# Kernel tuning notes

Hardware: AMD Instinct MI355X
Metric: run time of the kernel (lower is better)

The kernel has to match this reference:

```python
import jax, jax.numpy as jnp
import numpy as np

N_EMBD = 1024
HEADS = 16
HEAD_DIM = N_EMBD // HEADS


def setup_inputs() -> dict:
    key = jax.random.key(0)
    k1, k2 = jax.random.split(key)
    x = jax.random.normal(k1, (2, 2048, N_EMBD), dtype=jnp.float32)
    W_qkv = jax.random.normal(k2, (N_EMBD, 3 * N_EMBD), dtype=jnp.float32) * (N_EMBD ** -0.5)
    b_qkv = jnp.zeros((3 * N_EMBD,), dtype=jnp.float32)
    return {"x": x, "W_qkv": W_qkv, "b_qkv": b_qkv}


def reference(x, W_qkv, b_qkv):
    B, T, _ = x.shape
    qkv = x @ W_qkv + b_qkv                      # [B, T, 3*n_embd]
    q, k, v = jnp.split(qkv, 3, axis=-1)
    q = q.reshape(B, T, HEADS, HEAD_DIM)
    k = k.reshape(B, T, HEADS, HEAD_DIM)
    v = v.reshape(B, T, HEADS, HEAD_DIM)
    attn = jnp.einsum('bthd,bThd->bhtT', q, k) / jnp.sqrt(jnp.float32(HEAD_DIM))
    causal = jnp.tril(jnp.ones((T, T), dtype=bool))  # [T, T]
    attn = jnp.where(causal, attn, -jnp.inf)
    attn = jax.nn.softmax(attn, axis=-1)
    # dropout is identity in deterministic/eval mode (training=False)
    out = jnp.einsum('bhtT,bThd->bthd', attn, v).reshape(B, T, N_EMBD)
    return out
```

## Files before the change

### kernel.cpp

```cpp
#include <hip/hip_runtime.h>
#include <hip/hip_bf16.h>

#define BATCH 2
#define TSEQ  2048
#define NEMBD 1024
#define HEADS 16
#define HDIM  64

typedef short          bf16x8 __attribute__((ext_vector_type(8)));
typedef float          f32x4  __attribute__((ext_vector_type(4)));
typedef unsigned short u16;

__device__ __forceinline__ u16 f2bf(float f) {
  unsigned int u = __float_as_uint(f);
  u += 0x7fffu + ((u >> 16) & 1u);
  return (u16)(u >> 16);
}

__device__ __forceinline__ void gld16(const u16* g, u16* l) {
  __builtin_amdgcn_global_load_lds(
      (const __attribute__((address_space(1))) unsigned int*)g,
      (__attribute__((address_space(3))) unsigned int*)l, 16, 0, 0);
}

__global__ __launch_bounds__(256) void k_prep(const float* __restrict__ x,
                                              u16* __restrict__ xb,
                                              const float* __restrict__ w,
                                              u16* __restrict__ wt) {
  __shared__ float tile[32][33];
  const int t = threadIdx.x;
  if (blockIdx.x < 4096) {
    int i = blockIdx.x * 256 + t;
    float4 v = ((const float4*)x)[i];
    ushort4 o;
    o.x = f2bf(v.x); o.y = f2bf(v.y); o.z = f2bf(v.z); o.w = f2bf(v.w);
    ((ushort4*)xb)[i] = o;
    return;
  }
  const int bid = blockIdx.x - 4096;
  const int n0 = (bid % 96) * 32;
  const int k0 = (bid / 96) * 32;
  const int r  = t >> 3;
  const int c4 = (t & 7) * 4;
  float4 v = *(const float4*)(w + (size_t)(k0 + r) * 3072 + n0 + c4);
  tile[r][c4 + 0] = v.x; tile[r][c4 + 1] = v.y;
  tile[r][c4 + 2] = v.z; tile[r][c4 + 3] = v.w;
  __syncthreads();
  ushort4 o;
  o.x = f2bf(tile[c4 + 0][r]);
  o.y = f2bf(tile[c4 + 1][r]);
  o.z = f2bf(tile[c4 + 2][r]);
  o.w = f2bf(tile[c4 + 3][r]);
  *(ushort4*)(wt + (size_t)(n0 + r) * 1024 + k0 + c4) = o;
}

__global__ __launch_bounds__(256, 3) void k_qkv_gemm(
    const u16* __restrict__ xb, const u16* __restrict__ wt,
    const float* __restrict__ bias,
    u16* __restrict__ qb, u16* __restrict__ kbuf, u16* __restrict__ vt) {
  __shared__ u16 As[2][128 * 32];
  __shared__ u16 Bs[2][128 * 32];

  const int t    = threadIdx.x;
  const int wv   = t >> 6;
  const int lane = t & 63;
  const int m    = lane & 15;
  const int quad = lane >> 4;
  const int lin  = blockIdx.x;
  const int cp   = lin >> 5;
  const int rp   = ((lin & 7) << 2) | ((lin >> 3) & 3);
  const int row0 = rp * 128;
  const int col0 = cp * 128;
  const int wr   = (wv >> 1) * 64;
  const int wc   = (wv & 1) * 64;
  const int sec  = col0 >> 10;

  const int srow = wv * 32 + (lane >> 2);
  const int scol = (lane & 3) * 8;
  const u16* ag = xb + (size_t)(row0 + srow) * 1024 + scol;
  const u16* bg = wt + (size_t)(col0 + srow) * 1024 + scol;
  u16* al[2] = {&As[0][(wv * 32) * 32], &As[1][(wv * 32) * 32]};
  u16* bl[2] = {&Bs[0][(wv * 32) * 32], &Bs[1][(wv * 32) * 32]};

  f32x4 acc[4][4];
  const f32x4 zf = {0.f, 0.f, 0.f, 0.f};
  for (int i = 0; i < 4; ++i)
    for (int j = 0; j < 4; ++j) acc[i][j] = zf;

  gld16(ag,             al[0]);
  gld16(ag + 16 * 1024, al[0] + 16 * 32);
  gld16(bg,             bl[0]);
  gld16(bg + 16 * 1024, bl[0] + 16 * 32);
  __syncthreads();

  for (int kt = 0; kt < 32; ++kt) {
    const int b = kt & 1;
    const u16* Ab = &As[b][0];
    const u16* Bb = &Bs[b][0];

    if (kt + 1 < 32) {
      const int kk = (kt + 1) * 32;
      const int nb = b ^ 1;
      gld16(ag + kk,             al[nb]);
      gld16(ag + kk + 16 * 1024, al[nb] + 16 * 32);
      gld16(bg + kk,             bl[nb]);
      gld16(bg + kk + 16 * 1024, bl[nb] + 16 * 32);
    }

    bf16x8 af[4], bfr[4];
#pragma unroll
    for (int mt = 0; mt < 4; ++mt)
      af[mt] = *(const bf16x8*)(Ab + (wr + mt * 16 + m) * 32 + quad * 8);
#pragma unroll
    for (int nt = 0; nt < 4; ++nt)
      bfr[nt] = *(const bf16x8*)(Bb + (wc + nt * 16 + m) * 32 + quad * 8);

    if (sec < 2) {
#pragma unroll
      for (int i = 0; i < 4; ++i)
#pragma unroll
        for (int j = 0; j < 4; ++j)
          acc[i][j] = __builtin_amdgcn_mfma_f32_16x16x32_bf16(
              bfr[i], af[j], acc[i][j], 0, 0, 0);
    } else {
#pragma unroll
      for (int i = 0; i < 4; ++i)
#pragma unroll
        for (int j = 0; j < 4; ++j)
          acc[i][j] = __builtin_amdgcn_mfma_f32_16x16x32_bf16(
              af[i], bfr[j], acc[i][j], 0, 0, 0);
    }

    __syncthreads();
  }

  if (sec < 2) {
    u16* dst = (sec == 0) ? qb : kbuf;
    const float sc = (sec == 0) ? 0.125f : 1.0f;
#pragma unroll
    for (int i = 0; i < 4; ++i) {
      const int Cc0 = col0 + wc + i * 16 + quad * 4;
      const float4 bv = *(const float4*)(bias + Cc0);
      const int c0 = Cc0 & 1023;
      const int h  = c0 >> 6;
      const int d0 = c0 & 63;
#pragma unroll
      for (int j = 0; j < 4; ++j) {
        const int tg = row0 + wr + j * 16 + m;
        const int bh = (tg >> 11) * HEADS + h;
        const int tl = tg & 2047;
        ushort4 pk;
        pk.x = f2bf((acc[i][j][0] + bv.x) * sc);
        pk.y = f2bf((acc[i][j][1] + bv.y) * sc);
        pk.z = f2bf((acc[i][j][2] + bv.z) * sc);
        pk.w = f2bf((acc[i][j][3] + bv.w) * sc);
        *(ushort4*)(dst + ((size_t)bh * TSEQ + tl) * HDIM + d0) = pk;
      }
    }
  } else {
#pragma unroll
    for (int j = 0; j < 4; ++j) {
      const int Cc = col0 + wc + j * 16 + m;
      const float bv = bias[Cc];
      const int c = Cc & 1023;
      const int h = c >> 6;
      const int d = c & 63;
#pragma unroll
      for (int i = 0; i < 4; ++i) {
        const int Rbase = row0 + wr + i * 16 + quad * 4;
        const int bh = (Rbase >> 11) * HEADS + h;
        const int t0 = Rbase & 2047;
        ushort4 pk;
        pk.x = f2bf(acc[i][j][0] + bv);
        pk.y = f2bf(acc[i][j][1] + bv);
        pk.z = f2bf(acc[i][j][2] + bv);
        pk.w = f2bf(acc[i][j][3] + bv);
        *(ushort4*)(vt + (size_t)(bh * HDIM + d) * TSEQ + t0) = pk;
      }
    }
  }
}

__global__ __launch_bounds__(256, 4) void k_attn(
    const u16* __restrict__ qb, const u16* __restrict__ kbuf,
    const u16* __restrict__ vt, float* __restrict__ out) {
  __shared__ __align__(16) u16 Kb[2][4096];
  __shared__ __align__(16) u16 Vb[2][4096];
  __shared__ __align__(16) u16 pt[4][1024];

  const int t     = threadIdx.x;
  const int wv    = t >> 6;
  const int lane  = t & 63;
  const int m     = lane & 15;
  const int quad  = lane >> 4;
  const int bh    = blockIdx.x & 31;
  const int qtg   = 31 - (blockIdx.x >> 5);
  const int qbase = (qtg * 4 + wv) * 16;
  const int nkt   = qtg + 1;

  u16* pw = &pt[wv][0];
  const int mm = m & 7;

  const u16* qrow = qb + ((size_t)bh * TSEQ + qbase + m) * HDIM + quad * 8;
  bf16x8 aq0 = *(const bf16x8*)(qrow);
  bf16x8 aq1 = *(const bf16x8*)(qrow + 32);

  const int sr = wv * 16 + (lane >> 3);
  const int gs = (lane & 7) ^ (sr & 7);
  const u16* kg = kbuf + ((size_t)bh * TSEQ + sr) * HDIM + gs * 8;
  const u16* vg = vt + ((size_t)bh * HDIM + sr) * TSEQ + gs * 8;
  u16* klds[2] = {&Kb[0][wv * 16 * 64], &Kb[1][wv * 16 * 64]};
  u16* vlds[2] = {&Vb[0][wv * 16 * 64], &Vb[1][wv * 16 * 64]};

  const int swL = (quad ^ mm) * 8;
  const int swH = ((quad + 4) ^ mm) * 8;

  f32x4 o[4];
  const f32x4 zf = {0.f, 0.f, 0.f, 0.f};
  for (int nt = 0; nt < 4; ++nt) o[nt] = zf;
  float rsum = 0.f;
  const int qi = qbase + m;

  gld16(kg,            klds[0]);
  gld16(kg + 8 * HDIM, klds[0] + 8 * 64);
  gld16(vg,            vlds[0]);
  gld16(vg + 8 * TSEQ, vlds[0] + 8 * 64);
  __syncthreads();

  for (int kt = 0; kt < nkt; ++kt) {
    const int b = kt & 1;
    const u16* kb0 = &Kb[b][0];
    const u16* vb0 = &Vb[b][0];

    if (kt + 1 < nkt) {
      const int nb = (kt + 1) & 1;
      const u16* kgn = kg + (size_t)(kt + 1) * 64 * HDIM;
      const u16* vgn = vg + (kt + 1) * 64;
      gld16(kgn,            klds[nb]);
      gld16(kgn + 8 * HDIM, klds[nb] + 8 * 64);
      gld16(vgn,            vlds[nb]);
      gld16(vgn + 8 * TSEQ, vlds[nb] + 8 * 64);
    }

    f32x4 s[4];
    for (int nt = 0; nt < 4; ++nt) s[nt] = zf;
#pragma unroll
    for (int nt = 0; nt < 4; ++nt) {
      bf16x8 kf = *(const bf16x8*)(kb0 + (nt * 16 + m) * 64 + swL);
      s[nt] = __builtin_amdgcn_mfma_f32_16x16x32_bf16(kf, aq0, s[nt], 0, 0, 0);
    }
#pragma unroll
    for (int nt = 0; nt < 4; ++nt) {
      bf16x8 kf = *(const bf16x8*)(kb0 + (nt * 16 + m) * 64 + swH);
      s[nt] = __builtin_amdgcn_mfma_f32_16x16x32_bf16(kf, aq1, s[nt], 0, 0, 0);
    }

    bf16x8 vfL[4], vfH[4];
#pragma unroll
    for (int nt = 0; nt < 4; ++nt) {
      vfL[nt] = *(const bf16x8*)(vb0 + (nt * 16 + m) * 64 + swL);
      vfH[nt] = *(const bf16x8*)(vb0 + (nt * 16 + m) * 64 + swH);
    }

    if (kt == nkt - 1) {
      const int kb = kt * 64 + quad * 4;
#pragma unroll
      for (int nt = 0; nt < 4; ++nt)
#pragma unroll
        for (int rg = 0; rg < 4; ++rg)
          if (kb + nt * 16 + rg > qi) s[nt][rg] = -1e30f;
    }

#pragma unroll
    for (int nt = 0; nt < 4; ++nt) {
      float p0 = __expf(s[nt][0]), p1 = __expf(s[nt][1]);
      float p2 = __expf(s[nt][2]), p3 = __expf(s[nt][3]);
      rsum += (p0 + p1) + (p2 + p3);
      ushort4 pk = {f2bf(p0), f2bf(p1), f2bf(p2), f2bf(p3)};
      *(ushort4*)(pw + m * 64 + (((2 * nt + (quad >> 1)) ^ mm) * 8)
                  + (quad & 1) * 4) = pk;
    }
    bf16x8 bp0 = *(const bf16x8*)(pw + m * 64 + swL);
    bf16x8 bp1 = *(const bf16x8*)(pw + m * 64 + swH);

#pragma unroll
    for (int nt = 0; nt < 4; ++nt)
      o[nt] = __builtin_amdgcn_mfma_f32_16x16x32_bf16(vfL[nt], bp0, o[nt], 0, 0, 0);
#pragma unroll
    for (int nt = 0; nt < 4; ++nt)
      o[nt] = __builtin_amdgcn_mfma_f32_16x16x32_bf16(vfH[nt], bp1, o[nt], 0, 0, 0);

    __syncthreads();
  }

  rsum += __shfl_xor(rsum, 16);
  rsum += __shfl_xor(rsum, 32);
  const float inv = 1.0f / rsum;

  const int bb = bh >> 4;
  const int h  = bh & 15;
  float* ob = out + ((size_t)(bb * TSEQ + qi) * NEMBD + h * HDIM + quad * 4);
#pragma unroll
  for (int nt = 0; nt < 4; ++nt) {
    float4 st;
    st.x = o[nt][0] * inv; st.y = o[nt][1] * inv;
    st.z = o[nt][2] * inv; st.w = o[nt][3] * inv;
    *(float4*)(ob + nt * 16) = st;
  }
}

extern "C" void kernel_launch(void* const* d_in, const int* in_sizes, int n_in,
                              void* d_out, int out_size, void* d_ws, size_t ws_size,
                              hipStream_t stream) {
  (void)in_sizes; (void)n_in; (void)out_size; (void)ws_size;
  const float* x    = (const float*)d_in[0];
  const float* W    = (const float*)d_in[1];
  const float* bqkv = (const float*)d_in[2];
  float* out = (float*)d_out;

  u16* ws   = (u16*)d_ws;
  u16* qb   = ws;
  u16* kbuf = ws + 4194304;
  u16* vt   = ws + 2 * 4194304;
  u16* xb   = ws + 3 * 4194304;
  u16* wt   = ws + 4 * 4194304;

  hipLaunchKernelGGL(k_prep, dim3(7168), dim3(256), 0, stream, x, xb, W, wt);
  hipLaunchKernelGGL(k_qkv_gemm, dim3(768), dim3(256), 0, stream,
                     xb, wt, bqkv, qb, kbuf, vt);
  hipLaunchKernelGGL(k_attn, dim3(1024), dim3(256), 0, stream,
                     qb, kbuf, vt, out);
}
```

Baseline: 150.7 us.

## Single-buffer QKV GEMM staging and issue attention prefetch after LDS reads

The QKV GEMM drops its double-buffered LDS staging. Each k-step now loads its tile into a single buffer between two barriers, which halves LDS use and may allow more resident blocks, but the global loads no longer overlap the MFMA work. In the attention kernel, the prefetch of the next K/V tile is moved after the current tile's LDS fragment reads. This lets the score MFMAs start before the async loads are queued, and may also reduce LDS contention.

```diff
diff --git a/kernel.cpp b/kernel.cpp
--- a/kernel.cpp
+++ b/kernel.cpp
@@ -58,8 +58,8 @@
     const u16* __restrict__ xb, const u16* __restrict__ wt,
     const float* __restrict__ bias,
     u16* __restrict__ qb, u16* __restrict__ kbuf, u16* __restrict__ vt) {
-  __shared__ u16 As[2][128 * 32];
-  __shared__ u16 Bs[2][128 * 32];
+  __shared__ u16 As[128 * 32];
+  __shared__ u16 Bs[128 * 32];
 
   const int t    = threadIdx.x;
   const int wv   = t >> 6;
@@ -79,41 +79,30 @@
   const int scol = (lane & 3) * 8;
   const u16* ag = xb + (size_t)(row0 + srow) * 1024 + scol;
   const u16* bg = wt + (size_t)(col0 + srow) * 1024 + scol;
-  u16* al[2] = {&As[0][(wv * 32) * 32], &As[1][(wv * 32) * 32]};
-  u16* bl[2] = {&Bs[0][(wv * 32) * 32], &Bs[1][(wv * 32) * 32]};
+  u16* al = As + (wv * 32) * 32;
+  u16* bl = Bs + (wv * 32) * 32;
 
   f32x4 acc[4][4];
   const f32x4 zf = {0.f, 0.f, 0.f, 0.f};
   for (int i = 0; i < 4; ++i)
     for (int j = 0; j < 4; ++j) acc[i][j] = zf;
 
-  gld16(ag,             al[0]);
-  gld16(ag + 16 * 1024, al[0] + 16 * 32);
-  gld16(bg,             bl[0]);
-  gld16(bg + 16 * 1024, bl[0] + 16 * 32);
-  __syncthreads();
-
   for (int kt = 0; kt < 32; ++kt) {
-    const int b = kt & 1;
-    const u16* Ab = &As[b][0];
-    const u16* Bb = &Bs[b][0];
-
-    if (kt + 1 < 32) {
-      const int kk = (kt + 1) * 32;
-      const int nb = b ^ 1;
-      gld16(ag + kk,             al[nb]);
-      gld16(ag + kk + 16 * 1024, al[nb] + 16 * 32);
-      gld16(bg + kk,             bl[nb]);
-      gld16(bg + kk + 16 * 1024, bl[nb] + 16 * 32);
-    }
+    const int kk = kt * 32;
+    __syncthreads();
+    gld16(ag + kk,             al);
+    gld16(ag + kk + 16 * 1024, al + 16 * 32);
+    gld16(bg + kk,             bl);
+    gld16(bg + kk + 16 * 1024, bl + 16 * 32);
+    __syncthreads();
 
     bf16x8 af[4], bfr[4];
 #pragma unroll
     for (int mt = 0; mt < 4; ++mt)
-      af[mt] = *(const bf16x8*)(Ab + (wr + mt * 16 + m) * 32 + quad * 8);
+      af[mt] = *(const bf16x8*)(As + (wr + mt * 16 + m) * 32 + quad * 8);
 #pragma unroll
     for (int nt = 0; nt < 4; ++nt)
-      bfr[nt] = *(const bf16x8*)(Bb + (wc + nt * 16 + m) * 32 + quad * 8);
+      bfr[nt] = *(const bf16x8*)(Bs + (wc + nt * 16 + m) * 32 + quad * 8);
 
     if (sec < 2) {
 #pragma unroll
@@ -130,8 +119,6 @@
           acc[i][j] = __builtin_amdgcn_mfma_f32_16x16x32_bf16(
               af[i], bfr[j], acc[i][j], 0, 0, 0);
     }
-
-    __syncthreads();
   }
 
   if (sec < 2) {
@@ -232,6 +219,26 @@
     const u16* kb0 = &Kb[b][0];
     const u16* vb0 = &Vb[b][0];
 
+    f32x4 s[4];
+    for (int nt = 0; nt < 4; ++nt) s[nt] = zf;
+#pragma unroll
+    for (int nt = 0; nt < 4; ++nt) {
+      bf16x8 kf = *(const bf16x8*)(kb0 + (nt * 16 + m) * 64 + swL);
+      s[nt] = __builtin_amdgcn_mfma_f32_16x16x32_bf16(kf, aq0, s[nt], 0, 0, 0);
+    }
+#pragma unroll
+    for (int nt = 0; nt < 4; ++nt) {
+      bf16x8 kf = *(const bf16x8*)(kb0 + (nt * 16 + m) * 64 + swH);
+      s[nt] = __builtin_amdgcn_mfma_f32_16x16x32_bf16(kf, aq1, s[nt], 0, 0, 0);
+    }
+
+    bf16x8 vfL[4], vfH[4];
+#pragma unroll
+    for (int nt = 0; nt < 4; ++nt) {
+      vfL[nt] = *(const bf16x8*)(vb0 + (nt * 16 + m) * 64 + swL);
+      vfH[nt] = *(const bf16x8*)(vb0 + (nt * 16 + m) * 64 + swH);
+    }
+
     if (kt + 1 < nkt) {
       const int nb = (kt + 1) & 1;
       const u16* kgn = kg + (size_t)(kt + 1) * 64 * HDIM;
@@ -242,26 +249,6 @@
       gld16(vgn + 8 * TSEQ, vlds[nb] + 8 * 64);
     }
 
-    f32x4 s[4];
-    for (int nt = 0; nt < 4; ++nt) s[nt] = zf;
-#pragma unroll
-    for (int nt = 0; nt < 4; ++nt) {
-      bf16x8 kf = *(const bf16x8*)(kb0 + (nt * 16 + m) * 64 + swL);
-      s[nt] = __builtin_amdgcn_mfma_f32_16x16x32_bf16(kf, aq0, s[nt], 0, 0, 0);
-    }
-#pragma unroll
-    for (int nt = 0; nt < 4; ++nt) {
-      bf16x8 kf = *(const bf16x8*)(kb0 + (nt * 16 + m) * 64 + swH);
-      s[nt] = __builtin_amdgcn_mfma_f32_16x16x32_bf16(kf, aq1, s[nt], 0, 0, 0);
-    }
-
-    bf16x8 vfL[4], vfH[4];
-#pragma unroll
-    for (int nt = 0; nt < 4; ++nt) {
-      vfL[nt] = *(const bf16x8*)(vb0 + (nt * 16 + m) * 64 + swL);
-      vfH[nt] = *(const bf16x8*)(vb0 + (nt * 16 + m) * 64 + swH);
-    }
-
     if (kt == nkt - 1) {
       const int kb = kt * 64 + quad * 4;
 #pragma unroll
```

Measured after the change: 179.6 us. 19.2% more time.
